# Kernel optimization log

Hardware: AMD Instinct MI355X
Metric: run time of the kernel (lower is better)

The kernel has to match this reference:

```python
import jax, jax.numpy as jnp
import numpy as np
from jax import lax

GRID_SIZE = 5
SPLINE_ORDER = 3
N_COEF = GRID_SIZE + SPLINE_ORDER  # 8 b-spline basis functions per input
GRID_LO, GRID_HI = -1.0, 1.0


def _grid():
    h = (GRID_HI - GRID_LO) / GRID_SIZE
    return jnp.arange(-SPLINE_ORDER, GRID_SIZE + SPLINE_ORDER + 1, dtype=jnp.float32) * h + GRID_LO


def _bsplines(x):
    # x: [..., in] -> [..., in, N_COEF] via Cox-de Boor recursion (efficient-kan)
    grid = _grid()
    x = x[..., None]
    bases = ((x >= grid[:-1]) & (x < grid[1:])).astype(x.dtype)
    for j in range(1, SPLINE_ORDER + 1):
        bases = ((x - grid[:-(j + 1)]) / (grid[j:-1] - grid[:-(j + 1)]) * bases[..., :-1]
                 + (grid[j + 1:] - x) / (grid[j + 1:] - grid[1:-j]) * bases[..., 1:])
    return bases


def _kan_linear(x, base_w, spline_w):
    # x: [..., in]; base_w: [out, in]; spline_w: [out, in, N_COEF]
    base = jax.nn.silu(x) @ base_w.T
    b = _bsplines(x).reshape(x.shape[:-1] + (-1,))  # [..., in*N_COEF]
    return base + b @ spline_w.reshape(spline_w.shape[0], -1).T


def _kan_conv(x, base_w, spline_w):
    # x: [B, C, H, W]; 3x3 valid KAN convolution
    patches = lax.conv_general_dilated_patches(x, (3, 3), (1, 1), 'VALID')  # [B, C*9, H-2, W-2]
    p = patches.transpose(0, 2, 3, 1)  # [B, Ho, Wo, C*9]
    out = _kan_linear(p, base_w, spline_w)  # [B, Ho, Wo, out]
    return out.transpose(0, 3, 1, 2)


def _maxpool2(x):
    return lax.reduce_window(x, -jnp.inf, lax.max, (1, 1, 2, 2), (1, 1, 2, 2), 'VALID')


def setup_inputs() -> dict:
    key = jax.random.key(0)
    ks = jax.random.split(key, 12)
    B = 2048
    x = jax.random.uniform(ks[0], (B, 1, 28, 28), dtype=jnp.float32)
    s = 0.1
    return {
        'x': x,
        'bw1': jax.random.normal(ks[1], (5, 9), dtype=jnp.float32) * s,
        'sw1': jax.random.normal(ks[2], (5, 9, N_COEF), dtype=jnp.float32) * s,
        'bw2': jax.random.normal(ks[3], (5, 45), dtype=jnp.float32) * s,
        'sw2': jax.random.normal(ks[4], (5, 45, N_COEF), dtype=jnp.float32) * s,
        'bw3': jax.random.normal(ks[5], (2, 45), dtype=jnp.float32) * s,
        'sw3': jax.random.normal(ks[6], (2, 45, N_COEF), dtype=jnp.float32) * s,
        'w1': jax.random.normal(ks[7], (500, 162), dtype=jnp.float32) * 0.05,
        'b1': jnp.zeros((500,), dtype=jnp.float32),
        'w2': jax.random.normal(ks[8], (10, 500), dtype=jnp.float32) * 0.05,
        'b2': jnp.zeros((10,), dtype=jnp.float32),
    }


def reference(x, bw1, sw1, bw2, sw2, bw3, sw3, w1, b1, w2, b2):
    h = _kan_conv(x, bw1, sw1)       # [B, 5, 26, 26]
    h = _maxpool2(h)                 # [B, 5, 13, 13]
    h = _kan_conv(h, bw2, sw2)       # [B, 5, 11, 11]
    h = _kan_conv(h, bw3, sw3)       # [B, 2, 9, 9]
    h = h.reshape(h.shape[0], -1)    # [B, 162]
    h = jax.nn.relu(h @ w1.T + b1)   # [B, 500]
    return h @ w2.T + b2             # [B, 10]
```

## Files before the change

kernel.cpp:

```cpp
#include <hip/hip_runtime.h>


typedef _Float16 h2 __attribute__((ext_vector_type(2)));

__device__ __forceinline__ h2 u2h(unsigned int u) {
  union { unsigned int x; h2 h; } v; v.x = u; return v.h;
}
__device__ __forceinline__ unsigned short f2h_bits(float x) {
  union { _Float16 h; unsigned short u; } v; v.h = (_Float16)x; return v.u;
}
__device__ __forceinline__ float h2f(unsigned short u) {
  union { unsigned short u; _Float16 h; } v; v.u = u; return (float)v.h;
}
__device__ __forceinline__ unsigned int pack2h(float a, float b) {
  return (unsigned int)f2h_bits(a) | ((unsigned int)f2h_bits(b) << 16);
}
__device__ __forceinline__ float fdot2(h2 a, h2 b, float c) {
  return __builtin_amdgcn_fdot2(a, b, c, false);
}

__device__ __forceinline__ void featurize_regs(float v, uint4& bs, float& silu) {
  silu = v / (1.0f + __expf(-v));
  bs.x = 0u; bs.y = 0u; bs.z = 0u; bs.w = 0u;
  float u = fmaf(v, 2.5f, 5.5f);
  if (u >= 0.0f && u < 11.0f) {
    float tf = floorf(u);
    float f = u - tf, f2 = f * f, f3 = f2 * f, om = 1.0f - f;
    const float c6 = 1.0f / 6.0f;
    float w0 = om * om * om * c6;
    float w1 = (3.0f * f3 - 6.0f * f2 + 4.0f) * c6;
    float w2 = (-3.0f * f3 + 3.0f * f2 + 3.0f * f + 1.0f) * c6;
    float w3 = f3 * c6;
    unsigned long long w01 =
        (unsigned long long)f2h_bits(w0) |
        ((unsigned long long)f2h_bits(w1) << 16) |
        ((unsigned long long)f2h_bits(w2) << 32) |
        ((unsigned long long)f2h_bits(w3) << 48);
    int t = (int)tf;
    int s = 16 * t - 48;
    unsigned long long lo, hi;
    if (s >= 0) {
      lo = (s < 64) ? (w01 << s) : 0ull;
      hi = (s == 0) ? 0ull : ((s < 64) ? (w01 >> (64 - s)) : (w01 << (s - 64)));
    } else {
      lo = w01 >> (-s);
      hi = 0ull;
    }
    bs.x = (unsigned int)lo; bs.y = (unsigned int)(lo >> 32);
    bs.z = (unsigned int)hi; bs.w = (unsigned int)(hi >> 32);
  }
}

__global__ __launch_bounds__(256) void k_prep(
    const float* __restrict__ bw1, const float* __restrict__ sw1,
    const float* __restrict__ bw2, const float* __restrict__ sw2,
    const float* __restrict__ bw3, const float* __restrict__ sw3,
    const float* __restrict__ w1, const float* __restrict__ w2,
    unsigned int* __restrict__ V1s, float* __restrict__ V1b,
    unsigned int* __restrict__ V2s, float* __restrict__ V2b,
    unsigned int* __restrict__ V3s, float* __restrict__ V3b,
    unsigned int* __restrict__ W1p4, float* __restrict__ W2p) {
  int t = blockIdx.x * 256 + threadIdx.x;
  if (t < 180) {
    int p = t & 3, o = (t >> 2) % 5, in = t / 20;
    V1s[t] = pack2h(sw1[(o * 9 + in) * 8 + 2 * p], sw1[(o * 9 + in) * 8 + 2 * p + 1]);
  }
  if (t < 45)  { int o = t % 5, in = t / 5; V1b[t] = bw1[o * 9 + in]; }
  if (t < 900) {
    int p = t & 3, o = (t >> 2) % 5, in = t / 20;
    V2s[t] = pack2h(sw2[(o * 45 + in) * 8 + 2 * p], sw2[(o * 45 + in) * 8 + 2 * p + 1]);
  }
  if (t < 225) { int o = t % 5, in = t / 5; V2b[t] = bw2[o * 45 + in]; }
  if (t < 360) {
    int p = t & 3, o = (t >> 2) & 1, in = t / 8;
    V3s[t] = pack2h(sw3[(o * 45 + in) * 8 + 2 * p], sw3[(o * 45 + in) * 8 + 2 * p + 1]);
  }
  if (t < 90)  { int o = t % 2, in = t / 2; V3b[t] = bw3[o * 45 + in]; }
  if (t < 43008) {
    int j = t & 3, o = (t >> 2) & 511, g = t >> 11;
    int kp = g * 4 + j;
    W1p4[t] = (o < 500 && kp < 81)
                  ? pack2h(w1[o * 162 + 2 * kp], w1[o * 162 + 2 * kp + 1])
                  : 0u;
  }
  if (t < 5120) {
    int o = t >> 9, k = t & 511;
    W2p[t] = (k < 500) ? w2[o * 500 + k] : 0.0f;
  }
}

__global__ __launch_bounds__(64, 2) void k_fused(
    const float* __restrict__ x,
    const unsigned int* __restrict__ V1s, const float* __restrict__ V1b,
    const unsigned int* __restrict__ V2s, const float* __restrict__ V2b,
    const unsigned int* __restrict__ V3s, const float* __restrict__ V3b,
    const unsigned int* __restrict__ W1p4, const float* __restrict__ W2p,
    const float* __restrict__ b1, const float* __restrict__ b2,
    float* __restrict__ out) {
  __shared__ uint4 bas[845];
  __shared__ unsigned short slu16[848];
  float*        basF = (float*)bas;
  float*        h3f  = basF + 2048;
  unsigned int* hpk  = (unsigned int*)basF + 2560;
  const int b = blockIdx.x;
  const int lane = threadIdx.x;

  #pragma unroll 1
  for (int l = lane; l < 784; l += 64) {
    uint4 bs; float sl;
    featurize_regs(x[b * 784 + l], bs, sl);
    bas[l] = bs; slu16[l] = f2h_bits(sl);
  }

  float h1v[3][5];
  #pragma unroll 1
  for (int it = 0; it < 3; ++it) {
    int p = it * 64 + lane;
    if (p < 169) {
      int py = p / 13, px = p % 13;
      int r0 = py * 2, c0 = px * 2;
      float wacc[4][5];
      #pragma unroll
      for (int wi = 0; wi < 4; ++wi)
        #pragma unroll
        for (int o = 0; o < 5; ++o) wacc[wi][o] = 0.0f;
      #pragma unroll
      for (int r = 0; r < 4; ++r) {
        uint4 q[4]; float sl[4];
        #pragma unroll
        for (int c = 0; c < 4; ++c) {
          q[c]  = bas[(r0 + r) * 28 + c0 + c];
          sl[c] = h2f(slu16[(r0 + r) * 28 + c0 + c]);
        }
        #pragma unroll
        for (int c = 0; c < 4; ++c) {
          h2 a0 = u2h(q[c].x), a1 = u2h(q[c].y), a2 = u2h(q[c].z), a3 = u2h(q[c].w);
          #pragma unroll
          for (int dy = 0; dy < 2; ++dy) {
            #pragma unroll
            for (int dx = 0; dx < 2; ++dx) {
              int ky = r - dy, kx = c - dx;
              if (ky >= 0 && ky < 3 && kx >= 0 && kx < 3) {
                const unsigned int* wp = V1s + (ky * 3 + kx) * 20;
                const float* bp = V1b + (ky * 3 + kx) * 5;
                #pragma unroll
                for (int o = 0; o < 5; ++o) {
                  float acc = wacc[dy * 2 + dx][o];
                  acc = fdot2(a0, u2h(wp[o * 4 + 0]), acc);
                  acc = fdot2(a1, u2h(wp[o * 4 + 1]), acc);
                  acc = fdot2(a2, u2h(wp[o * 4 + 2]), acc);
                  acc = fdot2(a3, u2h(wp[o * 4 + 3]), acc);
                  wacc[dy * 2 + dx][o] = fmaf(sl[c], bp[o], acc);
                }
              }
            }
          }
        }
      }
      #pragma unroll
      for (int o = 0; o < 5; ++o)
        h1v[it][o] = fmaxf(fmaxf(wacc[0][o], wacc[1][o]),
                           fmaxf(wacc[2][o], wacc[3][o]));
    }
  }
  #pragma unroll 1
  for (int it = 0; it < 3; ++it) {
    int p = it * 64 + lane;
    if (p < 169) {
      #pragma unroll
      for (int o = 0; o < 5; ++o) {
        uint4 bs; float sl;
        featurize_regs(h1v[it][o], bs, sl);
        bas[o * 169 + p] = bs; slu16[o * 169 + p] = f2h_bits(sl);
      }
    }
  }

  float acc2[2][5];
  {
    #pragma unroll
    for (int ct = 0; ct < 2; ++ct)
      #pragma unroll
      for (int o = 0; o < 5; ++o) acc2[ct][o] = 0.0f;
    int pos0 = lane;
    int y0 = pos0 / 11, x0 = pos0 % 11;
    int pos1 = 64 + lane;
    int p1c = (pos1 < 121) ? pos1 : 120;
    int y1 = p1c / 11, x1 = p1c % 11;
    #pragma unroll 1
    for (int cky = 0; cky < 15; ++cky) {
      int c = cky / 3, ky = cky - c * 3;
      int ba0 = c * 169 + (y0 + ky) * 13 + x0;
      int ba1 = c * 169 + (y1 + ky) * 13 + x1;
      uint4 q00 = bas[ba0], q01 = bas[ba0 + 1], q02 = bas[ba0 + 2];
      uint4 q10 = bas[ba1], q11 = bas[ba1 + 1], q12 = bas[ba1 + 2];
      float s00 = h2f(slu16[ba0]), s01 = h2f(slu16[ba0 + 1]), s02 = h2f(slu16[ba0 + 2]);
      float s10 = h2f(slu16[ba1]), s11 = h2f(slu16[ba1 + 1]), s12 = h2f(slu16[ba1 + 2]);
      uint4 wq[15]; float wb[15];
      const uint4* wp4 = (const uint4*)(V2s + cky * 60);
      const float* bp  = V2b + cky * 15;
      #pragma unroll
      for (int i = 0; i < 15; ++i) { wq[i] = wp4[i]; wb[i] = bp[i]; }
      #pragma unroll
      for (int ct = 0; ct < 2; ++ct) {
        #pragma unroll
        for (int kx = 0; kx < 3; ++kx) {
          uint4 q = ct ? ((kx == 0) ? q10 : ((kx == 1) ? q11 : q12))
                       : ((kx == 0) ? q00 : ((kx == 1) ? q01 : q02));
          float sl = ct ? ((kx == 0) ? s10 : ((kx == 1) ? s11 : s12))
                        : ((kx == 0) ? s00 : ((kx == 1) ? s01 : s02));
          h2 a0 = u2h(q.x), a1 = u2h(q.y), a2 = u2h(q.z), a3 = u2h(q.w);
          #pragma unroll
          for (int o = 0; o < 5; ++o) {
            uint4 w = wq[kx * 5 + o];
            float a = acc2[ct][o];
            a = fdot2(a0, u2h(w.x), a);
            a = fdot2(a1, u2h(w.y), a);
            a = fdot2(a2, u2h(w.z), a);
            a = fdot2(a3, u2h(w.w), a);
            acc2[ct][o] = fmaf(sl, wb[kx * 5 + o], a);
          }
        }
      }
    }
  }
  #pragma unroll 1
  for (int ct = 0; ct < 2; ++ct) {
    int pos = ct * 64 + lane;
    if (pos < 121) {
      #pragma unroll
      for (int o = 0; o < 5; ++o) {
        uint4 bs; float sl;
        featurize_regs(acc2[ct][o], bs, sl);
        bas[o * 121 + pos] = bs; slu16[o * 121 + pos] = f2h_bits(sl);
      }
    }
  }

  float acc3[2][2];
  {
    acc3[0][0] = acc3[0][1] = acc3[1][0] = acc3[1][1] = 0.0f;
    int pos0 = lane;
    int y0 = pos0 / 9, x0 = pos0 % 9;
    int pos1 = 64 + lane;
    int p1c = (pos1 < 81) ? pos1 : 80;
    int y1 = p1c / 9, x1 = p1c % 9;
    #pragma unroll 1
    for (int cky = 0; cky < 15; ++cky) {
      int c = cky / 3, ky = cky - c * 3;
      int ba0 = c * 121 + (y0 + ky) * 11 + x0;
      int ba1 = c * 121 + (y1 + ky) * 11 + x1;
      uint4 q00 = bas[ba0], q01 = bas[ba0 + 1], q02 = bas[ba0 + 2];
      uint4 q10 = bas[ba1], q11 = bas[ba1 + 1], q12 = bas[ba1 + 2];
      float s00 = h2f(slu16[ba0]), s01 = h2f(slu16[ba0 + 1]), s02 = h2f(slu16[ba0 + 2]);
      float s10 = h2f(slu16[ba1]), s11 = h2f(slu16[ba1 + 1]), s12 = h2f(slu16[ba1 + 2]);
      uint4 wq[6]; float wb[6];
      const uint4* wp4 = (const uint4*)(V3s + cky * 24);
      const float* bp  = V3b + cky * 6;
      #pragma unroll
      for (int i = 0; i < 6; ++i) { wq[i] = wp4[i]; wb[i] = bp[i]; }
      #pragma unroll
      for (int ct = 0; ct < 2; ++ct) {
        #pragma unroll
        for (int kx = 0; kx < 3; ++kx) {
          uint4 q = ct ? ((kx == 0) ? q10 : ((kx == 1) ? q11 : q12))
                       : ((kx == 0) ? q00 : ((kx == 1) ? q01 : q02));
          float sl = ct ? ((kx == 0) ? s10 : ((kx == 1) ? s11 : s12))
                        : ((kx == 0) ? s00 : ((kx == 1) ? s01 : s02));
          h2 a0 = u2h(q.x), a1 = u2h(q.y), a2 = u2h(q.z), a3 = u2h(q.w);
          #pragma unroll
          for (int o = 0; o < 2; ++o) {
            uint4 w = wq[kx * 2 + o];
            float a = acc3[ct][o];
            a = fdot2(a0, u2h(w.x), a);
            a = fdot2(a1, u2h(w.y), a);
            a = fdot2(a2, u2h(w.z), a);
            a = fdot2(a3, u2h(w.w), a);
            acc3[ct][o] = fmaf(sl, wb[kx * 2 + o], a);
          }
        }
      }
    }
  }
  #pragma unroll 1
  for (int ct = 0; ct < 2; ++ct) {
    int pos = ct * 64 + lane;
    if (pos < 81) { h3f[pos] = acc3[ct][0]; h3f[81 + pos] = acc3[ct][1]; }
  }
  hpk[lane] = pack2h(h3f[2 * lane], h3f[2 * lane + 1]);
  {
    int i1 = 64 + lane;
    if (i1 < 84)
      hpk[i1] = (i1 < 81) ? pack2h(h3f[2 * i1], h3f[2 * i1 + 1]) : 0u;
  }

  float fa[8];
  #pragma unroll
  for (int i = 0; i < 8; ++i) fa[i] = 0.0f;
  {
    const uint4* hp4 = (const uint4*)hpk;
    const uint4* wbase = (const uint4*)W1p4 + lane;
    uint4 wA[8], wB[8];
    #pragma unroll
    for (int i = 0; i < 8; ++i) wA[i] = wbase[i * 64];
    #pragma unroll 1
    for (int g = 0; g < 21; g += 2) {
      if (g + 1 < 21) {
        const uint4* p = wbase + (g + 1) * 512;
        #pragma unroll
        for (int i = 0; i < 8; ++i) wB[i] = p[i * 64];
      }
      {
        uint4 hk = hp4[g];
        #pragma unroll
        for (int i = 0; i < 8; ++i) {
          float a = fa[i];
          a = fdot2(u2h(hk.x), u2h(wA[i].x), a);
          a = fdot2(u2h(hk.y), u2h(wA[i].y), a);
          a = fdot2(u2h(hk.z), u2h(wA[i].z), a);
          a = fdot2(u2h(hk.w), u2h(wA[i].w), a);
          fa[i] = a;
        }
      }
      if (g + 2 < 21) {
        const uint4* p = wbase + (g + 2) * 512;
        #pragma unroll
        for (int i = 0; i < 8; ++i) wA[i] = p[i * 64];
      }
      if (g + 1 < 21) {
        uint4 hk = hp4[g + 1];
        #pragma unroll
        for (int i = 0; i < 8; ++i) {
          float a = fa[i];
          a = fdot2(u2h(hk.x), u2h(wB[i].x), a);
          a = fdot2(u2h(hk.y), u2h(wB[i].y), a);
          a = fdot2(u2h(hk.z), u2h(wB[i].z), a);
          a = fdot2(u2h(hk.w), u2h(wB[i].w), a);
          fa[i] = a;
        }
      }
    }
  }
  #pragma unroll
  for (int i = 0; i < 8; ++i) {
    int o = lane + 64 * i;
    float bb = (o < 500) ? b1[o] : 0.0f;
    float v = fa[i] + bb;
    basF[o] = (v > 0.0f && o < 500) ? v : 0.0f;
  }

  float hv0, hv1, hv2, hv3, hv4, hv5, hv6, hv7;
  {
    const float4* hf = (const float4*)&basF[lane * 8];
    float4 ha = hf[0], hb = hf[1];
    hv0 = ha.x; hv1 = ha.y; hv2 = ha.z; hv3 = ha.w;
    hv4 = hb.x; hv5 = hb.y; hv6 = hb.z; hv7 = hb.w;
  }
  float acc10[10];
  #pragma unroll
  for (int o = 0; o < 10; ++o) {
    const float4* wp = (const float4*)&W2p[o * 512 + lane * 8];
    float4 w0 = wp[0], w1v = wp[1];
    float s = hv0 * w0.x + hv1 * w0.y + hv2 * w0.z + hv3 * w0.w;
    s += hv4 * w1v.x + hv5 * w1v.y + hv6 * w1v.z + hv7 * w1v.w;
    acc10[o] = s;
  }
  #pragma unroll
  for (int off = 32; off > 0; off >>= 1) {
    #pragma unroll
    for (int o = 0; o < 10; ++o) acc10[o] += __shfl_down(acc10[o], off);
  }
  if (lane == 0) {
    #pragma unroll
    for (int o = 0; o < 10; ++o) out[b * 10 + o] = acc10[o] + b2[o];
  }
}

extern "C" void kernel_launch(void* const* d_in, const int* in_sizes, int n_in,
                              void* d_out, int out_size, void* d_ws, size_t ws_size,
                              hipStream_t stream) {
  (void)in_sizes; (void)n_in; (void)out_size; (void)ws_size;
  const float* x   = (const float*)d_in[0];
  const float* bw1 = (const float*)d_in[1];
  const float* sw1 = (const float*)d_in[2];
  const float* bw2 = (const float*)d_in[3];
  const float* sw2 = (const float*)d_in[4];
  const float* bw3 = (const float*)d_in[5];
  const float* sw3 = (const float*)d_in[6];
  const float* w1  = (const float*)d_in[7];
  const float* b1  = (const float*)d_in[8];
  const float* w2  = (const float*)d_in[9];
  const float* b2  = (const float*)d_in[10];
  float* out = (float*)d_out;

  char* ws = (char*)d_ws;
  unsigned int* V1s  = (unsigned int*)(ws);
  float*        V1b  = (float*)(ws + 768);
  unsigned int* V2s  = (unsigned int*)(ws + 1024);
  float*        V2b  = (float*)(ws + 4672);
  unsigned int* V3s  = (unsigned int*)(ws + 5632);
  float*        V3b  = (float*)(ws + 7168);
  float*        W2p  = (float*)(ws + 7680);
  unsigned int* W1p4 = (unsigned int*)(ws + 28672);

  k_prep<<<168, 256, 0, stream>>>(bw1, sw1, bw2, sw2, bw3, sw3, w1, w2,
                                  V1s, V1b, V2s, V2b, V3s, V3b, W1p4, W2p);
  k_fused<<<2048, 64, 0, stream>>>(x, V1s, V1b, V2s, V2b, V3s, V3b,
                                   W1p4, W2p, b1, b2, out);
}
```

Measured before the change: 136.1 us.

## Split per-sample fused KAN network across two wavefronts with block barriers

Each sample's block grows from one 64-lane wavefront to 128 threads, so each thread handles half as many conv positions and FC outputs. Work per thread in every stage is halved, which should cut the serial per-block critical path and per-thread register use. In exchange it adds several __syncthreads barriers and a shared-memory cross-wave reduction for the final layer. Some lanes sit idle where position counts (169, 121, 81) do not fill 128 threads.

```diff
diff --git a/kernel.cpp b/kernel.cpp
--- a/kernel.cpp
+++ b/kernel.cpp
@@ -89,7 +89,7 @@
   }
 }
 
-__global__ __launch_bounds__(64, 2) void k_fused(
+__global__ __launch_bounds__(128, 4) void k_fused(
     const float* __restrict__ x,
     const unsigned int* __restrict__ V1s, const float* __restrict__ V1b,
     const unsigned int* __restrict__ V2s, const float* __restrict__ V2b,
@@ -99,23 +99,25 @@
     float* __restrict__ out) {
   __shared__ uint4 bas[845];
   __shared__ unsigned short slu16[848];
+  __shared__ float red[20];
   float*        basF = (float*)bas;
   float*        h3f  = basF + 2048;
   unsigned int* hpk  = (unsigned int*)basF + 2560;
   const int b = blockIdx.x;
-  const int lane = threadIdx.x;
+  const int tid = threadIdx.x;
 
   #pragma unroll 1
-  for (int l = lane; l < 784; l += 64) {
+  for (int l = tid; l < 784; l += 128) {
     uint4 bs; float sl;
     featurize_regs(x[b * 784 + l], bs, sl);
     bas[l] = bs; slu16[l] = f2h_bits(sl);
   }
-
-  float h1v[3][5];
+  __syncthreads();
+
+  float h1v[2][5];
   #pragma unroll 1
-  for (int it = 0; it < 3; ++it) {
-    int p = it * 64 + lane;
+  for (int it = 0; it < 2; ++it) {
+    int p = it * 128 + tid;
     if (p < 169) {
       int py = p / 13, px = p % 13;
       int r0 = py * 2, c0 = px * 2;
@@ -163,9 +165,10 @@
                            fmaxf(wacc[2][o], wacc[3][o]));
     }
   }
+  __syncthreads();
   #pragma unroll 1
-  for (int it = 0; it < 3; ++it) {
-    int p = it * 64 + lane;
+  for (int it = 0; it < 2; ++it) {
+    int p = it * 128 + tid;
     if (p < 169) {
       #pragma unroll
       for (int o = 0; o < 5; ++o) {
@@ -175,145 +178,115 @@
       }
     }
   }
-
-  float acc2[2][5];
+  __syncthreads();
+
+  float acc2[5];
   {
     #pragma unroll
-    for (int ct = 0; ct < 2; ++ct)
-      #pragma unroll
-      for (int o = 0; o < 5; ++o) acc2[ct][o] = 0.0f;
-    int pos0 = lane;
-    int y0 = pos0 / 11, x0 = pos0 % 11;
-    int pos1 = 64 + lane;
-    int p1c = (pos1 < 121) ? pos1 : 120;
-    int y1 = p1c / 11, x1 = p1c % 11;
+    for (int o = 0; o < 5; ++o) acc2[o] = 0.0f;
+    int pc = (tid < 121) ? tid : 120;
+    int y0 = pc / 11, x0 = pc % 11;
     #pragma unroll 1
     for (int cky = 0; cky < 15; ++cky) {
       int c = cky / 3, ky = cky - c * 3;
       int ba0 = c * 169 + (y0 + ky) * 13 + x0;
-      int ba1 = c * 169 + (y1 + ky) * 13 + x1;
       uint4 q00 = bas[ba0], q01 = bas[ba0 + 1], q02 = bas[ba0 + 2];
-      uint4 q10 = bas[ba1], q11 = bas[ba1 + 1], q12 = bas[ba1 + 2];
       float s00 = h2f(slu16[ba0]), s01 = h2f(slu16[ba0 + 1]), s02 = h2f(slu16[ba0 + 2]);
-      float s10 = h2f(slu16[ba1]), s11 = h2f(slu16[ba1 + 1]), s12 = h2f(slu16[ba1 + 2]);
       uint4 wq[15]; float wb[15];
       const uint4* wp4 = (const uint4*)(V2s + cky * 60);
       const float* bp  = V2b + cky * 15;
       #pragma unroll
       for (int i = 0; i < 15; ++i) { wq[i] = wp4[i]; wb[i] = bp[i]; }
       #pragma unroll
-      for (int ct = 0; ct < 2; ++ct) {
-        #pragma unroll
-        for (int kx = 0; kx < 3; ++kx) {
-          uint4 q = ct ? ((kx == 0) ? q10 : ((kx == 1) ? q11 : q12))
-                       : ((kx == 0) ? q00 : ((kx == 1) ? q01 : q02));
-          float sl = ct ? ((kx == 0) ? s10 : ((kx == 1) ? s11 : s12))
-                        : ((kx == 0) ? s00 : ((kx == 1) ? s01 : s02));
-          h2 a0 = u2h(q.x), a1 = u2h(q.y), a2 = u2h(q.z), a3 = u2h(q.w);
-          #pragma unroll
-          for (int o = 0; o < 5; ++o) {
-            uint4 w = wq[kx * 5 + o];
-            float a = acc2[ct][o];
-            a = fdot2(a0, u2h(w.x), a);
-            a = fdot2(a1, u2h(w.y), a);
-            a = fdot2(a2, u2h(w.z), a);
-            a = fdot2(a3, u2h(w.w), a);
-            acc2[ct][o] = fmaf(sl, wb[kx * 5 + o], a);
-          }
-        }
-      }
-    }
-  }
-  #pragma unroll 1
-  for (int ct = 0; ct < 2; ++ct) {
-    int pos = ct * 64 + lane;
-    if (pos < 121) {
-      #pragma unroll
-      for (int o = 0; o < 5; ++o) {
-        uint4 bs; float sl;
-        featurize_regs(acc2[ct][o], bs, sl);
-        bas[o * 121 + pos] = bs; slu16[o * 121 + pos] = f2h_bits(sl);
-      }
-    }
-  }
-
-  float acc3[2][2];
+      for (int kx = 0; kx < 3; ++kx) {
+        uint4 q = (kx == 0) ? q00 : ((kx == 1) ? q01 : q02);
+        float sl = (kx == 0) ? s00 : ((kx == 1) ? s01 : s02);
+        h2 a0 = u2h(q.x), a1 = u2h(q.y), a2 = u2h(q.z), a3 = u2h(q.w);
+        #pragma unroll
+        for (int o = 0; o < 5; ++o) {
+          uint4 w = wq[kx * 5 + o];
+          float a = acc2[o];
+          a = fdot2(a0, u2h(w.x), a);
+          a = fdot2(a1, u2h(w.y), a);
+          a = fdot2(a2, u2h(w.z), a);
+          a = fdot2(a3, u2h(w.w), a);
+          acc2[o] = fmaf(sl, wb[kx * 5 + o], a);
+        }
+      }
+    }
+  }
+  __syncthreads();
+  if (tid < 121) {
+    #pragma unroll
+    for (int o = 0; o < 5; ++o) {
+      uint4 bs; float sl;
+      featurize_regs(acc2[o], bs, sl);
+      bas[o * 121 + tid] = bs; slu16[o * 121 + tid] = f2h_bits(sl);
+    }
+  }
+  __syncthreads();
+
+  float acc3[2];
   {
-    acc3[0][0] = acc3[0][1] = acc3[1][0] = acc3[1][1] = 0.0f;
-    int pos0 = lane;
-    int y0 = pos0 / 9, x0 = pos0 % 9;
-    int pos1 = 64 + lane;
-    int p1c = (pos1 < 81) ? pos1 : 80;
-    int y1 = p1c / 9, x1 = p1c % 9;
+    acc3[0] = acc3[1] = 0.0f;
+    int pc = (tid < 81) ? tid : 80;
+    int y0 = pc / 9, x0 = pc % 9;
     #pragma unroll 1
     for (int cky = 0; cky < 15; ++cky) {
       int c = cky / 3, ky = cky - c * 3;
       int ba0 = c * 121 + (y0 + ky) * 11 + x0;
-      int ba1 = c * 121 + (y1 + ky) * 11 + x1;
       uint4 q00 = bas[ba0], q01 = bas[ba0 + 1], q02 = bas[ba0 + 2];
-      uint4 q10 = bas[ba1], q11 = bas[ba1 + 1], q12 = bas[ba1 + 2];
       float s00 = h2f(slu16[ba0]), s01 = h2f(slu16[ba0 + 1]), s02 = h2f(slu16[ba0 + 2]);
-      float s10 = h2f(slu16[ba1]), s11 = h2f(slu16[ba1 + 1]), s12 = h2f(slu16[ba1 + 2]);
       uint4 wq[6]; float wb[6];
       const uint4* wp4 = (const uint4*)(V3s + cky * 24);
       const float* bp  = V3b + cky * 6;
       #pragma unroll
       for (int i = 0; i < 6; ++i) { wq[i] = wp4[i]; wb[i] = bp[i]; }
       #pragma unroll
-      for (int ct = 0; ct < 2; ++ct) {
-        #pragma unroll
-        for (int kx = 0; kx < 3; ++kx) {
-          uint4 q = ct ? ((kx == 0) ? q10 : ((kx == 1) ? q11 : q12))
-                       : ((kx == 0) ? q00 : ((kx == 1) ? q01 : q02));
-          float sl = ct ? ((kx == 0) ? s10 : ((kx == 1) ? s11 : s12))
-                        : ((kx == 0) ? s00 : ((kx == 1) ? s01 : s02));
-          h2 a0 = u2h(q.x), a1 = u2h(q.y), a2 = u2h(q.z), a3 = u2h(q.w);
-          #pragma unroll
-          for (int o = 0; o < 2; ++o) {
-            uint4 w = wq[kx * 2 + o];
-            float a = acc3[ct][o];
-            a = fdot2(a0, u2h(w.x), a);
-            a = fdot2(a1, u2h(w.y), a);
-            a = fdot2(a2, u2h(w.z), a);
-            a = fdot2(a3, u2h(w.w), a);
-            acc3[ct][o] = fmaf(sl, wb[kx * 2 + o], a);
-          }
-        }
-      }
-    }
-  }
-  #pragma unroll 1
-  for (int ct = 0; ct < 2; ++ct) {
-    int pos = ct * 64 + lane;
-    if (pos < 81) { h3f[pos] = acc3[ct][0]; h3f[81 + pos] = acc3[ct][1]; }
-  }
-  hpk[lane] = pack2h(h3f[2 * lane], h3f[2 * lane + 1]);
-  {
-    int i1 = 64 + lane;
-    if (i1 < 84)
-      hpk[i1] = (i1 < 81) ? pack2h(h3f[2 * i1], h3f[2 * i1 + 1]) : 0u;
-  }
-
-  float fa[8];
+      for (int kx = 0; kx < 3; ++kx) {
+        uint4 q = (kx == 0) ? q00 : ((kx == 1) ? q01 : q02);
+        float sl = (kx == 0) ? s00 : ((kx == 1) ? s01 : s02);
+        h2 a0 = u2h(q.x), a1 = u2h(q.y), a2 = u2h(q.z), a3 = u2h(q.w);
+        #pragma unroll
+        for (int o = 0; o < 2; ++o) {
+          uint4 w = wq[kx * 2 + o];
+          float a = acc3[o];
+          a = fdot2(a0, u2h(w.x), a);
+          a = fdot2(a1, u2h(w.y), a);
+          a = fdot2(a2, u2h(w.z), a);
+          a = fdot2(a3, u2h(w.w), a);
+          acc3[o] = fmaf(sl, wb[kx * 2 + o], a);
+        }
+      }
+    }
+  }
+  __syncthreads();
+  if (tid < 81) { h3f[tid] = acc3[0]; h3f[81 + tid] = acc3[1]; }
+  __syncthreads();
+  if (tid < 84)
+    hpk[tid] = (tid < 81) ? pack2h(h3f[2 * tid], h3f[2 * tid + 1]) : 0u;
+  __syncthreads();
+
+  float fa[4];
   #pragma unroll
-  for (int i = 0; i < 8; ++i) fa[i] = 0.0f;
+  for (int i = 0; i < 4; ++i) fa[i] = 0.0f;
   {
     const uint4* hp4 = (const uint4*)hpk;
-    const uint4* wbase = (const uint4*)W1p4 + lane;
-    uint4 wA[8], wB[8];
-    #pragma unroll
-    for (int i = 0; i < 8; ++i) wA[i] = wbase[i * 64];
+    const uint4* wbase = (const uint4*)W1p4 + tid;
+    uint4 wA[4], wB[4];
+    #pragma unroll
+    for (int i = 0; i < 4; ++i) wA[i] = wbase[i * 128];
     #pragma unroll 1
     for (int g = 0; g < 21; g += 2) {
       if (g + 1 < 21) {
         const uint4* p = wbase + (g + 1) * 512;
         #pragma unroll
-        for (int i = 0; i < 8; ++i) wB[i] = p[i * 64];
+        for (int i = 0; i < 4; ++i) wB[i] = p[i * 128];
       }
       {
         uint4 hk = hp4[g];
         #pragma unroll
-        for (int i = 0; i < 8; ++i) {
+        for (int i = 0; i < 4; ++i) {
           float a = fa[i];
           a = fdot2(u2h(hk.x), u2h(wA[i].x), a);
           a = fdot2(u2h(hk.y), u2h(wA[i].y), a);
@@ -325,12 +298,12 @@
       if (g + 2 < 21) {
         const uint4* p = wbase + (g + 2) * 512;
         #pragma unroll
-        for (int i = 0; i < 8; ++i) wA[i] = p[i * 64];
+        for (int i = 0; i < 4; ++i) wA[i] = p[i * 128];
       }
       if (g + 1 < 21) {
         uint4 hk = hp4[g + 1];
         #pragma unroll
-        for (int i = 0; i < 8; ++i) {
+        for (int i = 0; i < 4; ++i) {
           float a = fa[i];
           a = fdot2(u2h(hk.x), u2h(wB[i].x), a);
           a = fdot2(u2h(hk.y), u2h(wB[i].y), a);
@@ -342,38 +315,36 @@
     }
   }
   #pragma unroll
-  for (int i = 0; i < 8; ++i) {
-    int o = lane + 64 * i;
+  for (int i = 0; i < 4; ++i) {
+    int o = tid + 128 * i;
     float bb = (o < 500) ? b1[o] : 0.0f;
     float v = fa[i] + bb;
     basF[o] = (v > 0.0f && o < 500) ? v : 0.0f;
   }
-
-  float hv0, hv1, hv2, hv3, hv4, hv5, hv6, hv7;
+  __syncthreads();
+
+  float acc10[10];
   {
-    const float4* hf = (const float4*)&basF[lane * 8];
-    float4 ha = hf[0], hb = hf[1];
-    hv0 = ha.x; hv1 = ha.y; hv2 = ha.z; hv3 = ha.w;
-    hv4 = hb.x; hv5 = hb.y; hv6 = hb.z; hv7 = hb.w;
-  }
-  float acc10[10];
-  #pragma unroll
-  for (int o = 0; o < 10; ++o) {
-    const float4* wp = (const float4*)&W2p[o * 512 + lane * 8];
-    float4 w0 = wp[0], w1v = wp[1];
-    float s = hv0 * w0.x + hv1 * w0.y + hv2 * w0.z + hv3 * w0.w;
-    s += hv4 * w1v.x + hv5 * w1v.y + hv6 * w1v.z + hv7 * w1v.w;
-    acc10[o] = s;
+    float4 ha = ((const float4*)basF)[tid];
+    #pragma unroll
+    for (int o = 0; o < 10; ++o) {
+      const float4* wp = (const float4*)&W2p[o * 512 + 4 * tid];
+      float4 w = wp[0];
+      acc10[o] = ha.x * w.x + ha.y * w.y + ha.z * w.z + ha.w * w.w;
+    }
   }
   #pragma unroll
   for (int off = 32; off > 0; off >>= 1) {
     #pragma unroll
     for (int o = 0; o < 10; ++o) acc10[o] += __shfl_down(acc10[o], off);
   }
-  if (lane == 0) {
-    #pragma unroll
-    for (int o = 0; o < 10; ++o) out[b * 10 + o] = acc10[o] + b2[o];
-  }
+  if ((tid & 63) == 0) {
+    int wid = tid >> 6;
+    #pragma unroll
+    for (int o = 0; o < 10; ++o) red[wid * 10 + o] = acc10[o];
+  }
+  __syncthreads();
+  if (tid < 10) out[b * 10 + tid] = red[tid] + red[10 + tid] + b2[tid];
 }
 
 extern "C" void kernel_launch(void* const* d_in, const int* in_sizes, int n_in,
@@ -405,6 +376,6 @@
 
   k_prep<<<168, 256, 0, stream>>>(bw1, sw1, bw2, sw2, bw3, sw3, w1, w2,
                                   V1s, V1b, V2s, V2b, V3s, V3b, W1p4, W2p);
-  k_fused<<<2048, 64, 0, stream>>>(x, V1s, V1b, V2s, V2b, V3s, V3b,
-                                   W1p4, W2p, b1, b2, out);
-}
+  k_fused<<<2048, 128, 0, stream>>>(x, V1s, V1b, V2s, V2b, V3s, V3b,
+                                    W1p4, W2p, b1, b2, out);
+}
```

After: 127.9 us. 1.06x faster.
